# Optimization experiments

Hardware: AMD Instinct MI355X
Metric: run time of the kernel (lower is better)

The kernel has to match this reference:

```python
import jax, jax.numpy as jnp
import numpy as np

N = 50000          # nodes
E = 400000         # edges
F = 128            # num_embeddings
NUM_TYPES = 100    # num_atoms (embedding vocab)
CUTOFF = 5.0
N_RBF = 20


def _silu(x):
    return x * jax.nn.sigmoid(x)


def setup_inputs() -> dict:
    key = jax.random.key(0)
    ks = jax.random.split(key, 16)
    pos = jax.random.normal(ks[0], (N, 3), dtype=jnp.float32) * 3.0
    z = jax.random.randint(ks[1], (N,), 0, NUM_TYPES)
    dst = jax.random.randint(ks[2], (E,), 0, N)
    # ensure src != dst so distances are nonzero
    src = (dst + 1 + jax.random.randint(ks[3], (E,), 0, N - 1)) % N
    def lin(k, fan_in, fan_out):
        kw, kb = jax.random.split(k)
        lim = 1.0 / np.sqrt(fan_in)
        W = jax.random.uniform(kw, (fan_out, fan_in), minval=-lim, maxval=lim, dtype=jnp.float32)
        b = jax.random.uniform(kb, (fan_out,), minval=-lim, maxval=lim, dtype=jnp.float32)
        return W, b
    emb_table = jax.random.normal(ks[4], (NUM_TYPES, F), dtype=jnp.float32)
    Wp1, bp1 = lin(ks[5], F, F)
    Wp2, bp2 = lin(ks[6], F, 3 * F)
    Ww, bw = lin(ks[7], N_RBF, 3 * F)
    Wu, bu = lin(ks[8], F, F)
    Wv, bv = lin(ks[9], F, F)
    Wu1, bu1 = lin(ks[10], 2 * F, F)
    Wu2, bu2 = lin(ks[11], F, 3 * F)
    return dict(pos=pos, emb_table=emb_table,
                Wp1=Wp1, bp1=bp1, Wp2=Wp2, bp2=bp2, Ww=Ww, bw=bw,
                Wu=Wu, bu=bu, Wv=Wv, bv=bv, Wu1=Wu1, bu1=bu1, Wu2=Wu2, bu2=bu2,
                z=z, src=src, dst=dst)


def painn_forward(pos, emb_table, Wp1, bp1, Wp2, bp2, Ww, bw, Wu, bu, Wv, bv,
                  Wu1, bu1, Wu2, bu2, z, src, dst):
    s = emb_table[z]                                  # [N,F] scalar features
    v = jnp.zeros((N, F, 3), dtype=s.dtype)          # equivariant features

    # ---- message block ----
    phi = _silu(s @ Wp1.T + bp1) @ Wp2.T + bp2       # [N,3F]
    rel = pos[dst] - pos[src]                        # [E,3]
    d = jnp.maximum(jnp.linalg.norm(rel, axis=-1), 1e-9)  # [E]
    n = jnp.arange(1, N_RBF + 1, dtype=jnp.float32)
    rbf = jnp.sin(n * jnp.pi * d[:, None] / CUTOFF) / d[:, None]   # [E,20]
    Wf = rbf @ Ww.T + bw                             # [E,3F]
    split = phi[src] * Wf                            # [E,3F] gated message
    ds = jax.ops.segment_sum(split[:, :F], dst, num_segments=N)    # [N,F]
    direction = rel / d[:, None]                     # [E,3]
    dv_e = v[src] * split[:, F:2 * F, None] + split[:, 2 * F:, None] * direction[:, None, :]  # [E,F,3]
    dv = jax.ops.segment_sum(dv_e, dst, num_segments=N)            # [N,F,3]
    s = s + ds
    v = v + dv

    # ---- update block ----
    U = jnp.einsum('nfc,gf->ngc', v, Wu) + bu[:, None]   # [N,F,3]
    V = jnp.einsum('nfc,gf->ngc', v, Wv) + bv[:, None]   # [N,F,3]
    Vn = jnp.linalg.norm(V, axis=-1)                     # [N,F]
    h = jnp.concatenate([s, Vn], axis=-1)                # [N,2F]
    a = _silu(h @ Wu1.T + bu1) @ Wu2.T + bu2             # [N,3F]
    dv2 = U * a[:, :F, None]                             # [N,F,3]
    ds2 = a[:, F:2 * F] + jnp.sum(U * V, axis=-1) * a[:, 2 * F:]   # [N,F]
    return s + ds2, v + dv2


def reference(pos, emb_table, Wp1, bp1, Wp2, bp2, Ww, bw, Wu, bu, Wv, bv,
              Wu1, bu1, Wu2, bu2, z, src, dst):
    return painn_forward(pos, emb_table, Wp1, bp1, Wp2, bp2, Ww, bw, Wu, bu,
                         Wv, bv, Wu1, bu1, Wu2, bu2, z, src, dst)
```

## Files before the change

### kernel.cpp

```cpp
#include <hip/hip_runtime.h>

#define NN 50000
#define EE 400000
#define FF 128
#define NRBF 20
#define MAXDEG 64
#define PI_OVER_CUT 0.6283185307179586f

typedef _Float16 h8 __attribute__((ext_vector_type(8)));
typedef float    f4 __attribute__((ext_vector_type(4)));

union pk32 { unsigned int u; _Float16 h[2]; };

__global__ __launch_bounds__(256) void k_bucket(const int* __restrict__ dst,
                                                int* __restrict__ counts,
                                                int* __restrict__ slots) {
    int e = blockIdx.x * 256 + threadIdx.x;
    if (e < EE) {
        int n = dst[e];
        int slot = atomicAdd(&counts[n], 1);
        if (slot < MAXDEG) slots[n * MAXDEG + slot] = e;
    }
}

__global__ __launch_bounds__(256) void k_wconv(
    const float* __restrict__ Wu, const float* __restrict__ Wv,
    const float* __restrict__ Wu1, const float* __restrict__ Wu2,
    const float* __restrict__ Wp1, const float* __restrict__ Wp2,
    const float* __restrict__ Ww, const float* __restrict__ bw,
    _Float16* __restrict__ Wuh, _Float16* __restrict__ Wvh,
    _Float16* __restrict__ Wu1h, _Float16* __restrict__ Wu2h,
    _Float16* __restrict__ Wp1h, _Float16* __restrict__ Wp2h,
    _Float16* __restrict__ Wwh32, int* __restrict__ counts)
{
    int i = blockIdx.x * 256 + threadIdx.x;
    if (i < NN) counts[i] = 0;
    if (i < 16384) { Wuh[i] = (_Float16)Wu[i]; Wvh[i] = (_Float16)Wv[i];
                     Wp1h[i] = (_Float16)Wp1[i]; }
    if (i < 32768) { Wu1h[i] = (_Float16)Wu1[i]; }
    if (i < 49152) { Wu2h[i] = (_Float16)Wu2[i]; Wp2h[i] = (_Float16)Wp2[i]; }
    if (i < 8192) {
        int col = i >> 5, k = i & 31;
        int sr = col < 128 ? col : col + 128;
        _Float16 v = (_Float16)0.f;
        if (k < 20)       v = (_Float16)Ww[sr * NRBF + k];
        else if (k == 20) v = (_Float16)bw[sr];
        Wwh32[i] = v;
    }
}

__global__ __launch_bounds__(256) void k_node_phi_mfma(
    const float* __restrict__ emb, const int* __restrict__ z,
    const _Float16* __restrict__ Wp1h, const float* __restrict__ bp1,
    const _Float16* __restrict__ Wp2h, const float* __restrict__ bp2,
    unsigned int* __restrict__ phi_pk, _Float16* __restrict__ s_h)
{
    __shared__ _Float16 Ss[32 * 128];
    __shared__ _Float16 H1s[32 * 128];

    const int t    = threadIdx.x;
    const int lane = t & 63;
    const int w    = t >> 6;
    const int lr   = lane & 15;
    const int lq   = lane >> 4;
    const int n0   = blockIdx.x * 32;
    const f4 z4 = {0.f, 0.f, 0.f, 0.f};

    for (int i = t; i < 512; i += 256) {
        int n = i >> 4, gr = i & 15;
        int nn = n0 + n; if (nn > NN - 1) nn = NN - 1;
        const float* sp = &emb[(size_t)z[nn] * FF + gr * 8];
        float4 aa = *(const float4*)sp;
        float4 bb = *(const float4*)(sp + 4);
        h8 hv;
        hv[0] = (_Float16)aa.x; hv[1] = (_Float16)aa.y;
        hv[2] = (_Float16)aa.z; hv[3] = (_Float16)aa.w;
        hv[4] = (_Float16)bb.x; hv[5] = (_Float16)bb.y;
        hv[6] = (_Float16)bb.z; hv[7] = (_Float16)bb.w;
        *(h8*)&Ss[(n * 16 + (gr ^ (n & 15))) * 8] = hv;
        *(h8*)&s_h[(size_t)nn * FF + gr * 8] = hv;
    }
    __syncthreads();

    f4 acc1[2][2];
    #pragma unroll
    for (int a = 0; a < 2; ++a)
        #pragma unroll
        for (int m = 0; m < 2; ++m) acc1[a][m] = z4;
    {
        const _Float16* bb = Wp1h + (size_t)lr * 128 + lq * 8;
        #pragma unroll
        for (int g2 = 0; g2 < 2; ++g2) {
            h8 bf[4];
            #pragma unroll
            for (int ks = 0; ks < 4; ++ks)
                bf[ks] = *(const h8*)(bb + ((2 * w + g2) * 16) * 128 + ks * 32);
            #pragma unroll
            for (int mt = 0; mt < 2; ++mt) {
                const int r = mt * 16 + lr;
                #pragma unroll
                for (int ks = 0; ks < 4; ++ks) {
                    h8 af = *(const h8*)&Ss[(r * 16 + ((ks * 4 + lq) ^ (r & 15))) * 8];
                    acc1[g2][mt] = __builtin_amdgcn_mfma_f32_16x16x32_f16(
                        af, bf[ks], acc1[g2][mt], 0, 0, 0);
                }
            }
        }
    }
    #pragma unroll
    for (int g2 = 0; g2 < 2; ++g2) {
        const int g = (2 * w + g2) * 16 + lr;
        const float b1 = bp1[g];
        #pragma unroll
        for (int mt = 0; mt < 2; ++mt)
            #pragma unroll
            for (int r = 0; r < 4; ++r) {
                float x = acc1[g2][mt][r] + b1;
                float y = x / (1.f + __expf(-x));
                int n = mt * 16 + lq * 4 + r;
                H1s[(n * 16 + ((g >> 3) ^ (n & 15))) * 8 + (g & 7)] = (_Float16)y;
            }
    }
    __syncthreads();

    f4 accS[2][2], accV[2][2];
    #pragma unroll
    for (int a = 0; a < 2; ++a)
        #pragma unroll
        for (int m = 0; m < 2; ++m) { accS[a][m] = z4; accV[a][m] = z4; }
    {
        const _Float16* bbs = Wp2h + (size_t)lr * 128 + lq * 8;
        const _Float16* bbv = Wp2h + (size_t)(256 + lr) * 128 + lq * 8;
        #pragma unroll
        for (int g2 = 0; g2 < 2; ++g2) {
            h8 bfs[4], bfv[4];
            #pragma unroll
            for (int ks = 0; ks < 4; ++ks) {
                bfs[ks] = *(const h8*)(bbs + ((2 * w + g2) * 16) * 128 + ks * 32);
                bfv[ks] = *(const h8*)(bbv + ((2 * w + g2) * 16) * 128 + ks * 32);
            }
            #pragma unroll
            for (int mt = 0; mt < 2; ++mt) {
                const int r = mt * 16 + lr;
                #pragma unroll
                for (int ks = 0; ks < 4; ++ks) {
                    h8 af = *(const h8*)&H1s[(r * 16 + ((ks * 4 + lq) ^ (r & 15))) * 8];
                    accS[g2][mt] = __builtin_amdgcn_mfma_f32_16x16x32_f16(
                        af, bfs[ks], accS[g2][mt], 0, 0, 0);
                    accV[g2][mt] = __builtin_amdgcn_mfma_f32_16x16x32_f16(
                        af, bfv[ks], accV[g2][mt], 0, 0, 0);
                }
            }
        }
    }
    #pragma unroll
    for (int g2 = 0; g2 < 2; ++g2) {
        const int g = (2 * w + g2) * 16 + lr;
        const float bsa = bp2[g], bva = bp2[256 + g];
        #pragma unroll
        for (int mt = 0; mt < 2; ++mt)
            #pragma unroll
            for (int r = 0; r < 4; ++r) {
                int n = mt * 16 + lq * 4 + r;
                int nn = n0 + n;
                if (nn < NN) {
                    pk32 pk;
                    pk.h[0] = (_Float16)(accS[g2][mt][r] + bsa);
                    pk.h[1] = (_Float16)(accV[g2][mt][r] + bva);
                    phi_pk[(size_t)nn * FF + g] = pk.u;
                }
            }
    }
}

__global__ __launch_bounds__(128) void k_edge_mfma(
    const float* __restrict__ pos,
    const _Float16* __restrict__ Wwh32,
    const int* __restrict__ src,
    const int* __restrict__ counts, const int* __restrict__ slots,
    const unsigned int* __restrict__ phi_pk,
    _Float16* __restrict__ s_h,
    _Float16* __restrict__ xg)
{
    __shared__ _Float16 A[2][16 * 32];
    __shared__ float dirs[2][16][4];
    __shared__ unsigned int wfi[2][16 * 66];

    const int t    = threadIdx.x;
    const int lane = t & 63;
    const int w    = t >> 6;
    const int lr   = lane & 15;
    const int lq   = lane >> 4;
    const int m    = lane & 15;
    const int ks   = lane >> 4;
    const int n    = blockIdx.x;
    const f4 z4 = {0.f, 0.f, 0.f, 0.f};

    h8 bf[8];
    #pragma unroll
    for (int js = 0; js < 8; ++js) {
        int col = (js < 4) ? (w * 64 + js * 16 + lr)
                           : (128 + w * 64 + (js - 4) * 16 + lr);
        bf[js] = *(const h8*)&Wwh32[(size_t)col * 32 + lq * 8];
    }

    const float px = pos[3 * n], py = pos[3 * n + 1], pz = pos[3 * n + 2];

    int deg = counts[n];
    deg = deg > MAXDEG ? MAXDEG : deg;

    const int gf = w * 64 + lane;
    const size_t gi = (size_t)n * FF + gf;
    float s_old = (float)s_h[gi];

    float acc_s = 0.f, av0 = 0.f, av1 = 0.f, av2 = 0.f;

    for (int t0 = 0; t0 < deg; t0 += 16) {
        const int degT = (deg - t0) < 16 ? (deg - t0) : 16;
        {
            int mc = (m < degT) ? m : 0;
            int e  = slots[n * MAXDEG + t0 + mc];
            int sI = src[e];
            float rx = px - pos[3 * sI];
            float ry = py - pos[3 * sI + 1];
            float rz = pz - pos[3 * sI + 2];
            float d = sqrtf(rx * rx + ry * ry + rz * rz);
            d = fmaxf(d, 1e-9f);
            float di = 1.f / d;
            if (lane < 16) {
                dirs[w][lane][0] = rx * di;
                dirs[w][lane][1] = ry * di;
                dirs[w][lane][2] = rz * di;
                dirs[w][lane][3] = __int_as_float(sI);
            }
            float vv[8];
            #pragma unroll
            for (int j = 0; j < 5; ++j)
                vv[j] = __sinf((float)(ks + 4 * j + 1) * PI_OVER_CUT * d) * di;
            vv[5] = (ks == 0) ? 1.0f : 0.f;
            vv[6] = 0.f; vv[7] = 0.f;
            #pragma unroll
            for (int j = 0; j < 8; ++j) {
                int k = ks + 4 * j;
                A[w][m * 32 + (((k >> 3) ^ (m & 3)) * 8) + (k & 7)] = (_Float16)vv[j];
            }
        }
        {
            h8 af = *(const h8*)&A[w][(lr * 4 + (lq ^ (lr & 3))) * 8];
            #pragma unroll
            for (int js = 0; js < 4; ++js) {
                f4 dd_s = __builtin_amdgcn_mfma_f32_16x16x32_f16(af, bf[js],     z4, 0, 0, 0);
                f4 dd_v = __builtin_amdgcn_mfma_f32_16x16x32_f16(af, bf[js + 4], z4, 0, 0, 0);
                #pragma unroll
                for (int r = 0; r < 4; ++r) {
                    pk32 pk;
                    pk.h[0] = (_Float16)dd_s[r];
                    pk.h[1] = (_Float16)dd_v[r];
                    wfi[w][(lq * 4 + r) * 66 + js * 16 + lr] = pk.u;
                }
            }
        }
        {
            unsigned int phr[16];
            #pragma unroll
            for (int mm = 0; mm < 16; ++mm) {
                int sim = __builtin_amdgcn_readfirstlane(
                              __float_as_int(dirs[w][mm][3]));
                phr[mm] = (mm < degT) ? phi_pk[(size_t)sim * FF + gf] : 0u;
            }
            #pragma unroll
            for (int mm = 0; mm < 16; ++mm) {
                if (mm < degT) {
                    pk32 ph, wfu;
                    ph.u  = phr[mm];
                    wfu.u = wfi[w][mm * 66 + lane];
                    float ps = (float)ph.h[0] * (float)wfu.h[0];
                    float pv = (float)ph.h[1] * (float)wfu.h[1];
                    acc_s += ps;
                    av0 = fmaf(pv, dirs[w][mm][0], av0);
                    av1 = fmaf(pv, dirs[w][mm][1], av1);
                    av2 = fmaf(pv, dirs[w][mm][2], av2);
                }
            }
        }
    }

    s_h[gi] = (_Float16)(s_old + acc_s);
    xg[((size_t)n * 3 + 0) * FF + gf] = (_Float16)av0;
    xg[((size_t)n * 3 + 1) * FF + gf] = (_Float16)av1;
    xg[((size_t)n * 3 + 2) * FF + gf] = (_Float16)av2;
}

__global__ __launch_bounds__(256) void k_update_mfma(
    const _Float16* __restrict__ xg, const _Float16* __restrict__ s_h,
    const _Float16* __restrict__ Wuh, const _Float16* __restrict__ Wvh,
    const _Float16* __restrict__ Wu1h, const _Float16* __restrict__ Wu2h,
    const float* __restrict__ bu, const float* __restrict__ bv,
    const float* __restrict__ bu1, const float* __restrict__ bu2,
    float* __restrict__ s_io, float* __restrict__ v_io)
{
    __shared__ _Float16 Xs[48 * 128];
    __shared__ _Float16 Hs[16 * 256];
    __shared__ _Float16 H1s[16 * 128];

    const int t    = threadIdx.x;
    const int lane = t & 63;
    const int w    = t >> 6;
    const int lr   = lane & 15;
    const int lq   = lane >> 4;
    const int n0   = blockIdx.x * 16;
    const f4 z4 = {0.f, 0.f, 0.f, 0.f};

    for (int i = t; i < 768; i += 256) {
        int row = i >> 4, gr = i & 15;
        int n = row & 15, c = row >> 4;
        int nn = n0 + n; if (nn > NN - 1) nn = NN - 1;
        uint4 d = *(const uint4*)&xg[((size_t)nn * 3 + c) * FF + gr * 8];
        *(uint4*)&Xs[(row * 16 + (gr ^ n)) * 8] = d;
    }
    {
        int n = t >> 4, gr = t & 15;
        int nn = n0 + n; if (nn > NN - 1) nn = NN - 1;
        uint4 d = *(const uint4*)&s_h[(size_t)nn * FF + gr * 8];
        *(uint4*)&Hs[(n * 32 + (gr ^ n)) * 8] = d;
    }
    __syncthreads();

    f4 accU[2][3], accV[2][3];
    #pragma unroll
    for (int a = 0; a < 2; ++a)
        #pragma unroll
        for (int c = 0; c < 3; ++c) { accU[a][c] = z4; accV[a][c] = z4; }

    {
        const _Float16* bb = Wuh + (size_t)lr * 128 + lq * 8;
        h8 bfr[2][4];
        #pragma unroll
        for (int g2 = 0; g2 < 2; ++g2)
            #pragma unroll
            for (int ks = 0; ks < 4; ++ks)
                bfr[g2][ks] = *(const h8*)(bb + ((2 * w + g2) * 16) * 128 + ks * 32);
        #pragma unroll
        for (int c = 0; c < 3; ++c) {
            const int rr = c * 16 + lr;
            h8 af[4];
            #pragma unroll
            for (int ks = 0; ks < 4; ++ks)
                af[ks] = *(const h8*)&Xs[(rr * 16 + ((ks * 4 + lq) ^ lr)) * 8];
            #pragma unroll
            for (int g2 = 0; g2 < 2; ++g2)
                #pragma unroll
                for (int ks = 0; ks < 4; ++ks)
                    accU[g2][c] = __builtin_amdgcn_mfma_f32_16x16x32_f16(
                        af[ks], bfr[g2][ks], accU[g2][c], 0, 0, 0);
        }
    }
    {
        const _Float16* bb = Wvh + (size_t)lr * 128 + lq * 8;
        h8 bfr[2][4];
        #pragma unroll
        for (int g2 = 0; g2 < 2; ++g2)
            #pragma unroll
            for (int ks = 0; ks < 4; ++ks)
                bfr[g2][ks] = *(const h8*)(bb + ((2 * w + g2) * 16) * 128 + ks * 32);
        #pragma unroll
        for (int c = 0; c < 3; ++c) {
            const int rr = c * 16 + lr;
            h8 af[4];
            #pragma unroll
            for (int ks = 0; ks < 4; ++ks)
                af[ks] = *(const h8*)&Xs[(rr * 16 + ((ks * 4 + lq) ^ lr)) * 8];
            #pragma unroll
            for (int g2 = 0; g2 < 2; ++g2)
                #pragma unroll
                for (int ks = 0; ks < 4; ++ks)
                    accV[g2][c] = __builtin_amdgcn_mfma_f32_16x16x32_f16(
                        af[ks], bfr[g2][ks], accV[g2][c], 0, 0, 0);
        }
    }

    float uvr[2][4];
    #pragma unroll
    for (int g2 = 0; g2 < 2; ++g2) {
        const int g = (2 * w + g2) * 16 + lr;
        const float bU = bu[g], bV = bv[g];
        #pragma unroll
        for (int r = 0; r < 4; ++r) {
            float Ux = accU[g2][0][r] + bU;
            float Uy = accU[g2][1][r] + bU;
            float Uz = accU[g2][2][r] + bU;
            float Vx = accV[g2][0][r] + bV;
            float Vy = accV[g2][1][r] + bV;
            float Vz = accV[g2][2][r] + bV;
            accU[g2][0][r] = Ux;
            accU[g2][1][r] = Uy;
            accU[g2][2][r] = Uz;
            uvr[g2][r] = Ux * Vx + Uy * Vy + Uz * Vz;
            float vn = sqrtf(Vx * Vx + Vy * Vy + Vz * Vz);
            int n = lq * 4 + r;
            int gr = 16 + (g >> 3);
            Hs[(n * 32 + (gr ^ n)) * 8 + (g & 7)] = (_Float16)vn;
        }
    }
    __syncthreads();

    f4 acc2[2];
    acc2[0] = z4; acc2[1] = z4;
    {
        const _Float16* bb = Wu1h + (size_t)lr * 256 + lq * 8;
        #pragma unroll
        for (int g2 = 0; g2 < 2; ++g2) {
            h8 bfr[8];
            #pragma unroll
            for (int ks = 0; ks < 8; ++ks)
                bfr[ks] = *(const h8*)(bb + ((2 * w + g2) * 16) * 256 + ks * 32);
            #pragma unroll
            for (int ks = 0; ks < 8; ++ks) {
                h8 af = *(const h8*)&Hs[(lr * 32 + ((ks * 4 + lq) ^ lr)) * 8];
                acc2[g2] = __builtin_amdgcn_mfma_f32_16x16x32_f16(
                    af, bfr[ks], acc2[g2], 0, 0, 0);
            }
        }
    }
    #pragma unroll
    for (int g2 = 0; g2 < 2; ++g2) {
        const int g = (2 * w + g2) * 16 + lr;
        const float b1 = bu1[g];
        #pragma unroll
        for (int r = 0; r < 4; ++r) {
            float x = acc2[g2][r] + b1;
            float y = x / (1.f + __expf(-x));
            int n = lq * 4 + r;
            H1s[(n * 16 + ((g >> 3) ^ n)) * 8 + (g & 7)] = (_Float16)y;
        }
    }
    __syncthreads();

    f4 acc3[3][2];
    #pragma unroll
    for (int a = 0; a < 3; ++a) { acc3[a][0] = z4; acc3[a][1] = z4; }
    {
        const _Float16* bb = Wu2h + (size_t)lr * 128 + lq * 8;
        #pragma unroll
        for (int ai = 0; ai < 3; ++ai)
            #pragma unroll
            for (int g2 = 0; g2 < 2; ++g2) {
                const int jt = ai * 8 + 2 * w + g2;
                h8 bfr[4];
                #pragma unroll
                for (int ks = 0; ks < 4; ++ks)
                    bfr[ks] = *(const h8*)(bb + (size_t)(jt * 16) * 128 + ks * 32);
                #pragma unroll
                for (int ks = 0; ks < 4; ++ks) {
                    h8 af = *(const h8*)&H1s[(lr * 16 + ((ks * 4 + lq) ^ lr)) * 8];
                    acc3[ai][g2] = __builtin_amdgcn_mfma_f32_16x16x32_f16(
                        af, bfr[ks], acc3[ai][g2], 0, 0, 0);
                }
            }
    }

    #pragma unroll
    for (int g2 = 0; g2 < 2; ++g2) {
        const int g = (2 * w + g2) * 16 + lr;
        const float b1 = bu2[g], b2 = bu2[128 + g], b3 = bu2[256 + g];
        #pragma unroll
        for (int r = 0; r < 4; ++r) {
            int n = lq * 4 + r;
            int nn = n0 + n;
            if (nn < NN) {
                float a1 = acc3[0][g2][r] + b1;
                float a2 = acc3[1][g2][r] + b2;
                float a3 = acc3[2][g2][r] + b3;
                size_t gi = (size_t)nn * FF + g;
                float s1 = (float)Hs[(n * 32 + ((g >> 3) ^ n)) * 8 + (g & 7)];
                s_io[gi] = s1 + a2 + uvr[g2][r] * a3;
                float vx = (float)Xs[((0 * 16 + n) * 16 + ((g >> 3) ^ n)) * 8 + (g & 7)];
                float vy = (float)Xs[((1 * 16 + n) * 16 + ((g >> 3) ^ n)) * 8 + (g & 7)];
                float vz = (float)Xs[((2 * 16 + n) * 16 + ((g >> 3) ^ n)) * 8 + (g & 7)];
                v_io[gi * 3 + 0] = vx + accU[g2][0][r] * a1;
                v_io[gi * 3 + 1] = vy + accU[g2][1][r] * a1;
                v_io[gi * 3 + 2] = vz + accU[g2][2][r] * a1;
            }
        }
    }
}

extern "C" void kernel_launch(void* const* d_in, const int* in_sizes, int n_in,
                              void* d_out, int out_size, void* d_ws, size_t ws_size,
                              hipStream_t stream)
{
    const float* pos = (const float*)d_in[0];
    const float* emb = (const float*)d_in[1];
    const float* Wp1 = (const float*)d_in[2];
    const float* bp1 = (const float*)d_in[3];
    const float* Wp2 = (const float*)d_in[4];
    const float* bp2 = (const float*)d_in[5];
    const float* Ww  = (const float*)d_in[6];
    const float* bw  = (const float*)d_in[7];
    const float* Wu  = (const float*)d_in[8];
    const float* bu  = (const float*)d_in[9];
    const float* Wv  = (const float*)d_in[10];
    const float* bv  = (const float*)d_in[11];
    const float* Wu1 = (const float*)d_in[12];
    const float* bu1 = (const float*)d_in[13];
    const float* Wu2 = (const float*)d_in[14];
    const float* bu2 = (const float*)d_in[15];
    const int* z   = (const int*)d_in[16];
    const int* src = (const int*)d_in[17];
    const int* dst = (const int*)d_in[18];

    float* s_io = (float*)d_out;
    float* v_io = (float*)d_out + (size_t)NN * FF;

    char* ws = (char*)d_ws;
    unsigned int* phi_pk = (unsigned int*)ws;
    _Float16* xg    = (_Float16*)(phi_pk + (size_t)NN * FF);
    _Float16* s_h   = xg + (size_t)NN * 3 * FF;
    _Float16* Wuh   = s_h + (size_t)NN * FF;
    _Float16* Wvh   = Wuh  + 128 * 128;
    _Float16* Wu1h  = Wvh  + 128 * 128;
    _Float16* Wu2h  = Wu1h + 128 * 256;
    _Float16* Wp1h  = Wu2h + 384 * 128;
    _Float16* Wp2h  = Wp1h + 128 * 128;
    _Float16* Wwh32 = Wp2h + 384 * 128;
    int* counts = (int*)(Wwh32 + 256 * 32);
    int* slots  = counts + NN;

    k_wconv <<<196, 256, 0, stream>>>(Wu, Wv, Wu1, Wu2, Wp1, Wp2, Ww, bw,
                                      Wuh, Wvh, Wu1h, Wu2h, Wp1h, Wp2h, Wwh32,
                                      counts);
    k_bucket<<<(EE + 255) / 256, 256, 0, stream>>>(dst, counts, slots);
    k_node_phi_mfma<<<(NN + 31) / 32, 256, 0, stream>>>(emb, z, Wp1h, bp1,
                                                        Wp2h, bp2,
                                                        phi_pk, s_h);
    k_edge_mfma<<<NN, 128, 0, stream>>>(pos, Wwh32, src, counts, slots,
                                        phi_pk, s_h, xg);
    k_update_mfma<<<(NN + 15) / 16, 256, 0, stream>>>(xg, s_h,
                                                      Wuh, Wvh, Wu1h, Wu2h,
                                                      bu, bv, bu1, bu2,
                                                      s_io, v_io);
}
```

Measured before the change: 379.3 us.

## Fuse edge bucketing into phi kernel and widen update kernel to 512 threads

Edge bucketing by destination moves into the node-phi kernel, with each thread handling one edge, so one kernel launch and its barrier are removed. The update kernel now runs 512 threads (8 waves) per 16-node block, with each wave owning a single 16-column group instead of two. This is meant to lower per-thread register pressure and raise occupancy. U values are kept as packed halves to save registers, which adds fp16 rounding to U in the v output and halves the work per wave.

```diff
diff --git a/kernel.cpp b/kernel.cpp
--- a/kernel.cpp
+++ b/kernel.cpp
@@ -11,17 +11,6 @@
 typedef float    f4 __attribute__((ext_vector_type(4)));
 
 union pk32 { unsigned int u; _Float16 h[2]; };
-
-__global__ __launch_bounds__(256) void k_bucket(const int* __restrict__ dst,
-                                                int* __restrict__ counts,
-                                                int* __restrict__ slots) {
-    int e = blockIdx.x * 256 + threadIdx.x;
-    if (e < EE) {
-        int n = dst[e];
-        int slot = atomicAdd(&counts[n], 1);
-        if (slot < MAXDEG) slots[n * MAXDEG + slot] = e;
-    }
-}
 
 __global__ __launch_bounds__(256) void k_wconv(
     const float* __restrict__ Wu, const float* __restrict__ Wv,
@@ -49,11 +38,13 @@
     }
 }
 
-__global__ __launch_bounds__(256) void k_node_phi_mfma(
+__global__ __launch_bounds__(256) void k_phi_bucket(
     const float* __restrict__ emb, const int* __restrict__ z,
     const _Float16* __restrict__ Wp1h, const float* __restrict__ bp1,
     const _Float16* __restrict__ Wp2h, const float* __restrict__ bp2,
-    unsigned int* __restrict__ phi_pk, _Float16* __restrict__ s_h)
+    unsigned int* __restrict__ phi_pk, _Float16* __restrict__ s_h,
+    const int* __restrict__ dst, int* __restrict__ counts,
+    int* __restrict__ slots)
 {
     __shared__ _Float16 Ss[32 * 128];
     __shared__ _Float16 H1s[32 * 128];
@@ -65,6 +56,15 @@
     const int lq   = lane >> 4;
     const int n0   = blockIdx.x * 32;
     const f4 z4 = {0.f, 0.f, 0.f, 0.f};
+
+    {
+        int e = blockIdx.x * 256 + t;
+        if (e < EE) {
+            int n = dst[e];
+            int slot = atomicAdd(&counts[n], 1);
+            if (slot < MAXDEG) slots[n * MAXDEG + slot] = e;
+        }
+    }
 
     for (int i = t; i < 512; i += 256) {
         int n = i >> 4, gr = i & 15;
@@ -291,7 +291,7 @@
     xg[((size_t)n * 3 + 2) * FF + gf] = (_Float16)av2;
 }
 
-__global__ __launch_bounds__(256) void k_update_mfma(
+__global__ __launch_bounds__(512, 8) void k_update_mfma(
     const _Float16* __restrict__ xg, const _Float16* __restrict__ s_h,
     const _Float16* __restrict__ Wuh, const _Float16* __restrict__ Wvh,
     const _Float16* __restrict__ Wu1h, const _Float16* __restrict__ Wu2h,
@@ -310,15 +310,16 @@
     const int lq   = lane >> 4;
     const int n0   = blockIdx.x * 16;
     const f4 z4 = {0.f, 0.f, 0.f, 0.f};
-
-    for (int i = t; i < 768; i += 256) {
+    const int g    = w * 16 + lr;
+
+    for (int i = t; i < 768; i += 512) {
         int row = i >> 4, gr = i & 15;
         int n = row & 15, c = row >> 4;
         int nn = n0 + n; if (nn > NN - 1) nn = NN - 1;
         uint4 d = *(const uint4*)&xg[((size_t)nn * 3 + c) * FF + gr * 8];
         *(uint4*)&Xs[(row * 16 + (gr ^ n)) * 8] = d;
     }
-    {
+    if (t < 256) {
         int n = t >> 4, gr = t & 15;
         int nn = n0 + n; if (nn > NN - 1) nn = NN - 1;
         uint4 d = *(const uint4*)&s_h[(size_t)nn * FF + gr * 8];
@@ -326,109 +327,98 @@
     }
     __syncthreads();
 
-    f4 accU[2][3], accV[2][3];
-    #pragma unroll
-    for (int a = 0; a < 2; ++a)
-        #pragma unroll
-        for (int c = 0; c < 3; ++c) { accU[a][c] = z4; accV[a][c] = z4; }
-
-    {
-        const _Float16* bb = Wuh + (size_t)lr * 128 + lq * 8;
-        h8 bfr[2][4];
-        #pragma unroll
-        for (int g2 = 0; g2 < 2; ++g2)
-            #pragma unroll
-            for (int ks = 0; ks < 4; ++ks)
-                bfr[g2][ks] = *(const h8*)(bb + ((2 * w + g2) * 16) * 128 + ks * 32);
+    f4 accU[3], accV[3];
+    #pragma unroll
+    for (int c = 0; c < 3; ++c) { accU[c] = z4; accV[c] = z4; }
+
+    {
+        const _Float16* bb = Wuh + (size_t)g * 128 + lq * 8;
+        h8 bfr[4];
+        #pragma unroll
+        for (int ks = 0; ks < 4; ++ks)
+            bfr[ks] = *(const h8*)(bb + ks * 32);
         #pragma unroll
         for (int c = 0; c < 3; ++c) {
             const int rr = c * 16 + lr;
-            h8 af[4];
-            #pragma unroll
-            for (int ks = 0; ks < 4; ++ks)
-                af[ks] = *(const h8*)&Xs[(rr * 16 + ((ks * 4 + lq) ^ lr)) * 8];
-            #pragma unroll
-            for (int g2 = 0; g2 < 2; ++g2)
-                #pragma unroll
-                for (int ks = 0; ks < 4; ++ks)
-                    accU[g2][c] = __builtin_amdgcn_mfma_f32_16x16x32_f16(
-                        af[ks], bfr[g2][ks], accU[g2][c], 0, 0, 0);
-        }
-    }
-    {
-        const _Float16* bb = Wvh + (size_t)lr * 128 + lq * 8;
-        h8 bfr[2][4];
-        #pragma unroll
-        for (int g2 = 0; g2 < 2; ++g2)
-            #pragma unroll
-            for (int ks = 0; ks < 4; ++ks)
-                bfr[g2][ks] = *(const h8*)(bb + ((2 * w + g2) * 16) * 128 + ks * 32);
+            #pragma unroll
+            for (int ks = 0; ks < 4; ++ks) {
+                h8 af = *(const h8*)&Xs[(rr * 16 + ((ks * 4 + lq) ^ lr)) * 8];
+                accU[c] = __builtin_amdgcn_mfma_f32_16x16x32_f16(
+                    af, bfr[ks], accU[c], 0, 0, 0);
+            }
+        }
+    }
+    {
+        const _Float16* bb = Wvh + (size_t)g * 128 + lq * 8;
+        h8 bfr[4];
+        #pragma unroll
+        for (int ks = 0; ks < 4; ++ks)
+            bfr[ks] = *(const h8*)(bb + ks * 32);
         #pragma unroll
         for (int c = 0; c < 3; ++c) {
             const int rr = c * 16 + lr;
-            h8 af[4];
-            #pragma unroll
-            for (int ks = 0; ks < 4; ++ks)
-                af[ks] = *(const h8*)&Xs[(rr * 16 + ((ks * 4 + lq) ^ lr)) * 8];
-            #pragma unroll
-            for (int g2 = 0; g2 < 2; ++g2)
-                #pragma unroll
-                for (int ks = 0; ks < 4; ++ks)
-                    accV[g2][c] = __builtin_amdgcn_mfma_f32_16x16x32_f16(
-                        af[ks], bfr[g2][ks], accV[g2][c], 0, 0, 0);
-        }
-    }
-
-    float uvr[2][4];
-    #pragma unroll
-    for (int g2 = 0; g2 < 2; ++g2) {
-        const int g = (2 * w + g2) * 16 + lr;
+            #pragma unroll
+            for (int ks = 0; ks < 4; ++ks) {
+                h8 af = *(const h8*)&Xs[(rr * 16 + ((ks * 4 + lq) ^ lr)) * 8];
+                accV[c] = __builtin_amdgcn_mfma_f32_16x16x32_f16(
+                    af, bfr[ks], accV[c], 0, 0, 0);
+            }
+        }
+    }
+
+    float uvr[4];
+    unsigned int upk[3][2];
+    {
         const float bU = bu[g], bV = bv[g];
         #pragma unroll
         for (int r = 0; r < 4; ++r) {
-            float Ux = accU[g2][0][r] + bU;
-            float Uy = accU[g2][1][r] + bU;
-            float Uz = accU[g2][2][r] + bU;
-            float Vx = accV[g2][0][r] + bV;
-            float Vy = accV[g2][1][r] + bV;
-            float Vz = accV[g2][2][r] + bV;
-            accU[g2][0][r] = Ux;
-            accU[g2][1][r] = Uy;
-            accU[g2][2][r] = Uz;
-            uvr[g2][r] = Ux * Vx + Uy * Vy + Uz * Vz;
+            float Ux = accU[0][r] + bU;
+            float Uy = accU[1][r] + bU;
+            float Uz = accU[2][r] + bU;
+            float Vx = accV[0][r] + bV;
+            float Vy = accV[1][r] + bV;
+            float Vz = accV[2][r] + bV;
+            accU[0][r] = Ux; accU[1][r] = Uy; accU[2][r] = Uz;
+            uvr[r] = Ux * Vx + Uy * Vy + Uz * Vz;
             float vn = sqrtf(Vx * Vx + Vy * Vy + Vz * Vz);
             int n = lq * 4 + r;
-            int gr = 16 + (g >> 3);
-            Hs[(n * 32 + (gr ^ n)) * 8 + (g & 7)] = (_Float16)vn;
-        }
+            Hs[(n * 32 + ((16 + (g >> 3)) ^ n)) * 8 + (g & 7)] = (_Float16)vn;
+        }
+        #pragma unroll
+        for (int c = 0; c < 3; ++c)
+            #pragma unroll
+            for (int rp = 0; rp < 2; ++rp) {
+                pk32 p;
+                p.h[0] = (_Float16)accU[c][2 * rp];
+                p.h[1] = (_Float16)accU[c][2 * rp + 1];
+                upk[c][rp] = p.u;
+            }
     }
     __syncthreads();
 
-    f4 acc2[2];
-    acc2[0] = z4; acc2[1] = z4;
-    {
-        const _Float16* bb = Wu1h + (size_t)lr * 256 + lq * 8;
-        #pragma unroll
-        for (int g2 = 0; g2 < 2; ++g2) {
-            h8 bfr[8];
-            #pragma unroll
-            for (int ks = 0; ks < 8; ++ks)
-                bfr[ks] = *(const h8*)(bb + ((2 * w + g2) * 16) * 256 + ks * 32);
-            #pragma unroll
-            for (int ks = 0; ks < 8; ++ks) {
-                h8 af = *(const h8*)&Hs[(lr * 32 + ((ks * 4 + lq) ^ lr)) * 8];
-                acc2[g2] = __builtin_amdgcn_mfma_f32_16x16x32_f16(
-                    af, bfr[ks], acc2[g2], 0, 0, 0);
-            }
-        }
-    }
-    #pragma unroll
-    for (int g2 = 0; g2 < 2; ++g2) {
-        const int g = (2 * w + g2) * 16 + lr;
+    f4 acc2 = z4;
+    {
+        const _Float16* bb = Wu1h + (size_t)g * 256 + lq * 8;
+        #pragma unroll
+        for (int half = 0; half < 2; ++half) {
+            h8 bfr[4];
+            #pragma unroll
+            for (int ks = 0; ks < 4; ++ks)
+                bfr[ks] = *(const h8*)(bb + (half * 4 + ks) * 32);
+            #pragma unroll
+            for (int ks = 0; ks < 4; ++ks) {
+                const int kk = half * 4 + ks;
+                h8 af = *(const h8*)&Hs[(lr * 32 + ((kk * 4 + lq) ^ lr)) * 8];
+                acc2 = __builtin_amdgcn_mfma_f32_16x16x32_f16(
+                    af, bfr[ks], acc2, 0, 0, 0);
+            }
+        }
+    }
+    {
         const float b1 = bu1[g];
         #pragma unroll
         for (int r = 0; r < 4; ++r) {
-            float x = acc2[g2][r] + b1;
+            float x = acc2[r] + b1;
             float y = x / (1.f + __expf(-x));
             int n = lq * 4 + r;
             H1s[(n * 16 + ((g >> 3) ^ n)) * 8 + (g & 7)] = (_Float16)y;
@@ -436,50 +426,49 @@
     }
     __syncthreads();
 
-    f4 acc3[3][2];
-    #pragma unroll
-    for (int a = 0; a < 3; ++a) { acc3[a][0] = z4; acc3[a][1] = z4; }
-    {
-        const _Float16* bb = Wu2h + (size_t)lr * 128 + lq * 8;
-        #pragma unroll
-        for (int ai = 0; ai < 3; ++ai)
-            #pragma unroll
-            for (int g2 = 0; g2 < 2; ++g2) {
-                const int jt = ai * 8 + 2 * w + g2;
-                h8 bfr[4];
-                #pragma unroll
-                for (int ks = 0; ks < 4; ++ks)
-                    bfr[ks] = *(const h8*)(bb + (size_t)(jt * 16) * 128 + ks * 32);
-                #pragma unroll
-                for (int ks = 0; ks < 4; ++ks) {
-                    h8 af = *(const h8*)&H1s[(lr * 16 + ((ks * 4 + lq) ^ lr)) * 8];
-                    acc3[ai][g2] = __builtin_amdgcn_mfma_f32_16x16x32_f16(
-                        af, bfr[ks], acc3[ai][g2], 0, 0, 0);
-                }
-            }
-    }
-
-    #pragma unroll
-    for (int g2 = 0; g2 < 2; ++g2) {
-        const int g = (2 * w + g2) * 16 + lr;
+    f4 acc3[3];
+    #pragma unroll
+    for (int ai = 0; ai < 3; ++ai) {
+        acc3[ai] = z4;
+        const _Float16* bb = Wu2h + (size_t)(ai * 128 + g) * 128 + lq * 8;
+        h8 bfr[4];
+        #pragma unroll
+        for (int ks = 0; ks < 4; ++ks)
+            bfr[ks] = *(const h8*)(bb + ks * 32);
+        #pragma unroll
+        for (int ks = 0; ks < 4; ++ks) {
+            h8 af = *(const h8*)&H1s[(lr * 16 + ((ks * 4 + lq) ^ lr)) * 8];
+            acc3[ai] = __builtin_amdgcn_mfma_f32_16x16x32_f16(
+                af, bfr[ks], acc3[ai], 0, 0, 0);
+        }
+    }
+
+    {
         const float b1 = bu2[g], b2 = bu2[128 + g], b3 = bu2[256 + g];
         #pragma unroll
         for (int r = 0; r < 4; ++r) {
             int n = lq * 4 + r;
             int nn = n0 + n;
             if (nn < NN) {
-                float a1 = acc3[0][g2][r] + b1;
-                float a2 = acc3[1][g2][r] + b2;
-                float a3 = acc3[2][g2][r] + b3;
+                float a1 = acc3[0][r] + b1;
+                float a2 = acc3[1][r] + b2;
+                float a3 = acc3[2][r] + b3;
                 size_t gi = (size_t)nn * FF + g;
                 float s1 = (float)Hs[(n * 32 + ((g >> 3) ^ n)) * 8 + (g & 7)];
-                s_io[gi] = s1 + a2 + uvr[g2][r] * a3;
+                s_io[gi] = s1 + a2 + uvr[r] * a3;
+                pk32 p0, p1, p2;
+                p0.u = upk[0][r >> 1];
+                p1.u = upk[1][r >> 1];
+                p2.u = upk[2][r >> 1];
+                float Ux = (float)p0.h[r & 1];
+                float Uy = (float)p1.h[r & 1];
+                float Uz = (float)p2.h[r & 1];
                 float vx = (float)Xs[((0 * 16 + n) * 16 + ((g >> 3) ^ n)) * 8 + (g & 7)];
                 float vy = (float)Xs[((1 * 16 + n) * 16 + ((g >> 3) ^ n)) * 8 + (g & 7)];
                 float vz = (float)Xs[((2 * 16 + n) * 16 + ((g >> 3) ^ n)) * 8 + (g & 7)];
-                v_io[gi * 3 + 0] = vx + accU[g2][0][r] * a1;
-                v_io[gi * 3 + 1] = vy + accU[g2][1][r] * a1;
-                v_io[gi * 3 + 2] = vz + accU[g2][2][r] * a1;
+                v_io[gi * 3 + 0] = vx + Ux * a1;
+                v_io[gi * 3 + 1] = vy + Uy * a1;
+                v_io[gi * 3 + 2] = vz + Uz * a1;
             }
         }
     }
@@ -529,13 +518,12 @@
     k_wconv <<<196, 256, 0, stream>>>(Wu, Wv, Wu1, Wu2, Wp1, Wp2, Ww, bw,
                                       Wuh, Wvh, Wu1h, Wu2h, Wp1h, Wp2h, Wwh32,
                                       counts);
-    k_bucket<<<(EE + 255) / 256, 256, 0, stream>>>(dst, counts, slots);
-    k_node_phi_mfma<<<(NN + 31) / 32, 256, 0, stream>>>(emb, z, Wp1h, bp1,
-                                                        Wp2h, bp2,
-                                                        phi_pk, s_h);
+    k_phi_bucket<<<(NN + 31) / 32, 256, 0, stream>>>(emb, z, Wp1h, bp1,
+                                                     Wp2h, bp2, phi_pk, s_h,
+                                                     dst, counts, slots);
     k_edge_mfma<<<NN, 128, 0, stream>>>(pos, Wwh32, src, counts, slots,
                                         phi_pk, s_h, xg);
-    k_update_mfma<<<(NN + 15) / 16, 256, 0, stream>>>(xg, s_h,
+    k_update_mfma<<<(NN + 15) / 16, 512, 0, stream>>>(xg, s_h,
                                                       Wuh, Wvh, Wu1h, Wu2h,
                                                       bu, bv, bu1, bu2,
                                                       s_io, v_io);
```

Result: no change. 386.1 us (+1.8%).
